# Performance work log

Hardware: AMD Instinct MI355X
Metric: run time of the kernel (lower is better)

Reference implementation:

```python
import jax, jax.numpy as jnp
import numpy as np

DIM = 192
HEADS = 6
POS_DIM = 12  # (dim//4)//4
EPS = 1e-5


def _ln(x, g, b):
    m = jnp.mean(x, -1, keepdims=True)
    v = jnp.var(x, -1, keepdims=True)
    return (x - m) / jnp.sqrt(v + EPS) * g + b


def setup_inputs() -> dict:
    key = jax.random.key(0)
    ks = jax.random.split(key, 20)
    B_, N = 256, 256
    s = 0.02
    inp = {
        "x": jax.random.normal(ks[0], (B_, N, DIM), jnp.float32),
        "mask": jax.random.normal(ks[1], (64, N, N), jnp.float32),
        "w_qkv": jax.random.normal(ks[2], (DIM, 3 * DIM), jnp.float32) * s,
        "b_qkv": jnp.zeros((3 * DIM,), jnp.float32),
        "w_proj": jax.random.normal(ks[3], (DIM, DIM), jnp.float32) * s,
        "b_proj": jnp.zeros((DIM,), jnp.float32),
        "pw0": jax.random.normal(ks[4], (2, POS_DIM), jnp.float32) * s,
        "pb0": jnp.zeros((POS_DIM,), jnp.float32),
        "g1": jnp.ones((POS_DIM,), jnp.float32),
        "be1": jnp.zeros((POS_DIM,), jnp.float32),
        "w1": jax.random.normal(ks[5], (POS_DIM, POS_DIM), jnp.float32) * s,
        "b1": jnp.zeros((POS_DIM,), jnp.float32),
        "g2": jnp.ones((POS_DIM,), jnp.float32),
        "be2": jnp.zeros((POS_DIM,), jnp.float32),
        "w2": jax.random.normal(ks[6], (POS_DIM, POS_DIM), jnp.float32) * s,
        "b2": jnp.zeros((POS_DIM,), jnp.float32),
        "g3": jnp.ones((POS_DIM,), jnp.float32),
        "be3": jnp.zeros((POS_DIM,), jnp.float32),
        "w3": jax.random.normal(ks[7], (POS_DIM, HEADS), jnp.float32) * s,
        "b3": jnp.zeros((HEADS,), jnp.float32),
        "H": 16,
        "W": 16,
    }
    return inp


def reference(x, mask, w_qkv, b_qkv, w_proj, b_proj, pw0, pb0, g1, be1, w1, b1,
              g2, be2, w2, b2, g3, be3, w3, b3, H, W):
    B_, N, C = x.shape
    d = C // HEADS
    scale = d ** (-0.5)
    qkv = (x @ w_qkv + b_qkv).reshape(B_, N, 3, HEADS, d)
    q, k, v = qkv[:, :, 0], qkv[:, :, 1], qkv[:, :, 2]  # [B_, N, h, d]
    attn = jnp.einsum('bnhd,bmhd->bhnm', q * scale, k)

    # dynamic position bias: MLP over relative coordinate offsets
    ph = jnp.arange(1 - H, H)
    pw = jnp.arange(1 - W, W)
    biases = jnp.stack(jnp.meshgrid(ph, pw, indexing='ij')).reshape(2, -1).T.astype(x.dtype)  # [(2H-1)(2W-1), 2]
    pos = biases @ pw0 + pb0
    pos = jax.nn.relu(_ln(pos, g1, be1)) @ w1 + b1
    pos = jax.nn.relu(_ln(pos, g2, be2)) @ w2 + b2
    pos = jax.nn.relu(_ln(pos, g3, be3)) @ w3 + b3  # [(2H-1)(2W-1), heads]

    coords = jnp.stack(jnp.meshgrid(jnp.arange(H), jnp.arange(W), indexing='ij')).reshape(2, -1)  # [2, N]
    rel = coords[:, :, None] - coords[:, None, :]  # [2, N, N]
    rpi = (rel[0] + H - 1) * (2 * W - 1) + (rel[1] + W - 1)  # [N, N]
    rpb = pos[rpi]  # gather -> [N, N, heads]
    attn = attn + jnp.transpose(rpb, (2, 0, 1))[None]

    nP = mask.shape[0]
    attn = attn.reshape(B_ // nP, nP, HEADS, N, N) + mask[None, :, None]
    attn = jax.nn.softmax(attn.reshape(B_, HEADS, N, N), axis=-1)

    out = jnp.einsum('bhnm,bmhd->bnhd', attn, v).reshape(B_, N, C)
    out = out @ w_proj + b_proj
    return out
```

## Files before the change

### kernel.cpp

```cpp
#include <hip/hip_runtime.h>
#include <hip/hip_bf16.h>
#include <math.h>

typedef __bf16 bf16;
typedef __bf16 bf16x8 __attribute__((ext_vector_type(8)));
typedef __bf16 bf16x4 __attribute__((ext_vector_type(4)));
typedef float  f32x4  __attribute__((ext_vector_type(4)));
typedef float  f32x16 __attribute__((ext_vector_type(16)));
typedef _Float16 f16x8 __attribute__((ext_vector_type(8)));

#define MFMA(a, b, c)   __builtin_amdgcn_mfma_f32_16x16x32_bf16((a), (b), (c), 0, 0, 0)
#define MFMA32(a, b, c) __builtin_amdgcn_mfma_f32_32x32x16_bf16((a), (b), (c), 0, 0, 0)
#define LOG2E 1.4426950408889634f

union U8 { unsigned u[4]; bf16x8 v; };

__global__ void precast_kernel(const float* __restrict__ w_qkv,
                               const float* __restrict__ w_proj,
                               bf16* __restrict__ wqT, bf16* __restrict__ wpT) {
  int idx = blockIdx.x * 256 + threadIdx.x;
  if (idx < 576 * 192) {
    int c = idx / 192, k = idx % 192;
    wqT[idx] = (bf16)w_qkv[k * 576 + c];
  } else {
    int i2 = idx - 576 * 192;
    if (i2 < 192 * 192) {
      int c = i2 / 192, k = i2 % 192;
      wpT[i2] = (bf16)w_proj[k * 192 + c];
    }
  }
}

__global__ void pos_mlp_kernel(
    const float* __restrict__ pw0, const float* __restrict__ pb0,
    const float* __restrict__ g1,  const float* __restrict__ be1,
    const float* __restrict__ w1,  const float* __restrict__ b1,
    const float* __restrict__ g2,  const float* __restrict__ be2,
    const float* __restrict__ w2,  const float* __restrict__ b2,
    const float* __restrict__ g3,  const float* __restrict__ be3,
    const float* __restrict__ w3,  const float* __restrict__ b3,
    float* __restrict__ pos_out) {
  int i = blockIdx.x * blockDim.x + threadIdx.x;
  if (i >= 961) return;
  float bh = (float)(i / 31) - 15.0f;
  float bw = (float)(i % 31) - 15.0f;
  float xv[12];
#pragma unroll
  for (int j = 0; j < 12; j++) xv[j] = bh * pw0[j] + bw * pw0[12 + j] + pb0[j];
  const float* G[3]  = {g1, g2, g3};
  const float* BE[3] = {be1, be2, be3};
  const float* W[3]  = {w1, w2, w3};
  const float* BB[3] = {b1, b2, b3};
#pragma unroll
  for (int s = 0; s < 3; s++) {
    float m = 0.f;
#pragma unroll
    for (int j = 0; j < 12; j++) m += xv[j];
    m *= (1.0f / 12.0f);
    float v = 0.f;
#pragma unroll
    for (int j = 0; j < 12; j++) { float d = xv[j] - m; v += d * d; }
    v *= (1.0f / 12.0f);
    float inv = 1.0f / sqrtf(v + 1e-5f);
    float y[12];
#pragma unroll
    for (int j = 0; j < 12; j++) {
      float t = (xv[j] - m) * inv * G[s][j] + BE[s][j];
      y[j] = t > 0.f ? t : 0.f;
    }
    int oc = (s == 2) ? 6 : 12;
    float on[12];
    for (int c = 0; c < oc; c++) {
      float acc = BB[s][c];
#pragma unroll
      for (int j = 0; j < 12; j++) acc += y[j] * W[s][j * oc + c];
      on[c] = acc;
    }
    for (int c = 0; c < 12; c++) xv[c] = (c < oc) ? on[c] : 0.f;
  }
  for (int hh = 0; hh < 6; hh++) pos_out[hh * 961 + i] = xv[hh];
}

__global__ void pos32_build_kernel(const float* __restrict__ posg,
                                   bf16* __restrict__ pos32g) {
  int rd = blockIdx.x, h = blockIdx.y;
  int t = threadIdx.x;
  for (int e = t; e < 512; e += 256) {
    int L = e >> 3, j = e & 7;
    int qh = L & 15;
    int hi = L >> 5;
    int idx = rd * 31 + qh - ((j & 3) + 8 * (j >> 2) + 4 * hi) + 15;
    pos32g[((h * 31 + rd) * 64 + L) * 8 + j] = (bf16)(posg[h * 961 + idx] * LOG2E);
  }
}

__global__ __launch_bounds__(256) void maskprep_kernel(
    const float* __restrict__ mask, _Float16* __restrict__ maskp) {
  size_t e = ((size_t)blockIdx.x * 256 + threadIdx.x) * 2;
  int j  = (int)(e & 15);
  int L  = (int)((e >> 4) & 63);
  int mt = (int)((e >> 10) & 7);
  int qt = (int)((e >> 13) & 7);
  int s  = (int)(e >> 16);
  int q  = qt * 32 + (L & 31);
  int m  = mt * 32 + 16 * (j >> 3) + 8 * ((j >> 2) & 1) + 4 * (L >> 5) + (j & 3);
  const float* src = mask + ((size_t)s * 256 + q) * 256 + m;
  maskp[e]     = (_Float16)(src[0] * LOG2E);
  maskp[e + 1] = (_Float16)(src[1] * LOG2E);
}

#define SMEM_G (192 * 200 * 2)

__global__ __launch_bounds__(256) void qkv_gemm_kernel(
    const float* __restrict__ x, const bf16* __restrict__ wqT,
    const float* __restrict__ b_qkv, bf16* __restrict__ qw,
    bf16* __restrict__ kw, bf16* __restrict__ vwT) {
  extern __shared__ char smem[];
  bf16* wt = (bf16*)smem;
  const int tid = threadIdx.x;
  const int lane = tid & 63, w = tid >> 6;
  const int cI = lane & 15, gI = lane >> 4;
  const int row0 = blockIdx.x * 128 + w * 32;
  const int b = blockIdx.x >> 1;
  const float QSCALE = 0.17677669529663687f * LOG2E;

  bf16x8 afr[2][6];
#pragma unroll
  for (int rt = 0; rt < 2; rt++) {
#pragma unroll
    for (int kk = 0; kk < 6; kk++) {
      const float* p = x + (size_t)(row0 + rt * 16 + cI) * 192 + kk * 32 + gI * 8;
      float4 f0 = *(const float4*)p;
      float4 f1 = *(const float4*)(p + 4);
      bf16x8 a;
      a[0] = (bf16)f0.x; a[1] = (bf16)f0.y; a[2] = (bf16)f0.z; a[3] = (bf16)f0.w;
      a[4] = (bf16)f1.x; a[5] = (bf16)f1.y; a[6] = (bf16)f1.z; a[7] = (bf16)f1.w;
      afr[rt][kk] = a;
    }
  }

#pragma unroll
  for (int mat = 0; mat < 3; mat++) {
    __syncthreads();
#pragma unroll
    for (int it = 0; it < 18; it++) {
      int idx = it * 256 + tid;
      int c = idx / 24, ch = idx % 24;
      bf16x8 v8 = *(const bf16x8*)(wqT + (size_t)(mat * 192 + c) * 192 + ch * 8);
      *(bf16x8*)(wt + c * 200 + ch * 8) = v8;
    }
    __syncthreads();
#pragma unroll
    for (int ct = 0; ct < 12; ct++) {
      bf16x8 wfr[6];
#pragma unroll
      for (int kk = 0; kk < 6; kk++)
        wfr[kk] = *(const bf16x8*)(wt + (ct * 16 + cI) * 200 + kk * 32 + gI * 8);
      if (mat < 2) {
        f32x4 bv4 = *(const f32x4*)(b_qkv + mat * 192 + ct * 16 + gI * 4);
        bf16* dst = (mat == 0) ? qw : kw;
#pragma unroll
        for (int rt = 0; rt < 2; rt++) {
          f32x4 acc = {0.f, 0.f, 0.f, 0.f};
#pragma unroll
          for (int kk = 0; kk < 6; kk++) acc = MFMA(wfr[kk], afr[rt][kk], acc);
          int n = (row0 + rt * 16 + cI) & 255;
          int c0 = ct * 16 + gI * 4;
          int h = c0 >> 5, d0 = c0 & 31;
          bf16x4 o4;
          if (mat == 0) {
#pragma unroll
            for (int r = 0; r < 4; r++) o4[r] = (bf16)((acc[r] + bv4[r]) * QSCALE);
          } else {
#pragma unroll
            for (int r = 0; r < 4; r++) o4[r] = (bf16)(acc[r] + bv4[r]);
          }
          *(bf16x4*)(dst + ((size_t)(b * 6 + h) * 256 + n) * 32 + d0) = o4;
        }
      } else {
        float bv = b_qkv[384 + ct * 16 + cI];
        int c = ct * 16 + cI, h = c >> 5, d = c & 31;
#pragma unroll
        for (int rt = 0; rt < 2; rt++) {
          f32x4 acc = {0.f, 0.f, 0.f, 0.f};
#pragma unroll
          for (int kk = 0; kk < 6; kk++) acc = MFMA(afr[rt][kk], wfr[kk], acc);
          int n0 = ((row0 + rt * 16) & 255) + gI * 4;
          bf16x4 o4;
#pragma unroll
          for (int r = 0; r < 4; r++) o4[r] = (bf16)(acc[r] + bv);
          *(bf16x4*)(vwT + ((size_t)(b * 6 + h) * 32 + d) * 256 + n0) = o4;
        }
      }
    }
  }
}

__global__ __launch_bounds__(256, 4) void attn_kernel(
    const bf16* __restrict__ qw, const bf16* __restrict__ kw,
    const bf16* __restrict__ vwT, const _Float16* __restrict__ maskp,
    const bf16* __restrict__ pos32g, bf16* __restrict__ ctx) {
  const int tid = threadIdx.x;
  const int bid = blockIdx.x;
  const int s_ = bid & 63, j_ = bid >> 6;
  const int g_ = j_ & 3, h = j_ >> 2;
  const int b = g_ * 64 + s_;

  const bf16* qb = qw  + (size_t)(b * 6 + h) * 8192;
  const bf16* kb = kw  + (size_t)(b * 6 + h) * 8192;
  const bf16* vb = vwT + (size_t)(b * 6 + h) * 8192;
  const bf16* pg = pos32g + (size_t)h * (31 * 512);

  const int lane = tid & 63, w = tid >> 6;
  const int q5 = lane & 31, hi = lane >> 5;

  bf16x8 qf[2][2];
#pragma unroll
  for (int sub = 0; sub < 2; sub++) {
    int qa = w * 64 + sub * 32 + q5;
    qf[sub][0] = *(const bf16x8*)(qb + qa * 32 + hi * 8);
    qf[sub][1] = *(const bf16x8*)(qb + qa * 32 + 16 + hi * 8);
  }

  f32x16 o[2];
  float l[2], mr[2];
#pragma unroll
  for (int sub = 0; sub < 2; sub++) {
#pragma unroll
    for (int r = 0; r < 16; r++) o[sub][r] = 0.f;
    l[sub] = 0.f; mr[sub] = -3.0e38f;
  }

  for (int mt = 0; mt < 8; mt++) {
    const int m0 = mt * 32;
    bf16x8 kf0 = *(const bf16x8*)(kb + (m0 + q5) * 32 + hi * 8);
    bf16x8 kf1 = *(const bf16x8*)(kb + (m0 + q5) * 32 + 16 + hi * 8);
    const bf16* vrow = vb + q5 * 256 + m0 + 4 * hi;
    bf16x4 v00 = *(const bf16x4*)(vrow);
    bf16x4 v01 = *(const bf16x4*)(vrow + 8);
    bf16x4 v10 = *(const bf16x4*)(vrow + 16);
    bf16x4 v11 = *(const bf16x4*)(vrow + 24);
    bf16x8 vf0, vf1;
#pragma unroll
    for (int j2 = 0; j2 < 4; j2++) {
      vf0[j2] = v00[j2]; vf0[4 + j2] = v01[j2];
      vf1[j2] = v10[j2]; vf1[4 + j2] = v11[j2];
    }

#pragma unroll
    for (int sub = 0; sub < 2; sub++) {
      const int qa = w * 64 + sub * 32 + q5;
      const int rn = qa >> 4;
      const int rd0 = rn - 2 * mt + 15;
      bf16x8 plo = *(const bf16x8*)(pg + ((rd0)*64 + lane) * 8);
      bf16x8 phi = *(const bf16x8*)(pg + ((rd0 - 1) * 64 + lane) * 8);
      const _Float16* mrow =
          maskp + ((((size_t)s_ * 8 + (w * 2 + sub)) * 8 + mt) * 64 + lane) * 16;
      f16x8 mk0 = *(const f16x8*)(mrow);
      f16x8 mk1 = *(const f16x8*)(mrow + 8);

      f32x16 sa;
#pragma unroll
      for (int r = 0; r < 16; r++) sa[r] = 0.f;
      __builtin_amdgcn_s_setprio(1);
      sa = MFMA32(kf0, qf[sub][0], sa);
      sa = MFMA32(kf1, qf[sub][1], sa);
      __builtin_amdgcn_s_setprio(0);

#pragma unroll
      for (int r = 0; r < 8; r++)  sa[r] += (float)mk0[r] + (float)plo[r];
#pragma unroll
      for (int r = 8; r < 16; r++) sa[r] += (float)mk1[r - 8] + (float)phi[r - 8];

      float t = sa[0];
#pragma unroll
      for (int r = 1; r < 16; r++) t = fmaxf(t, sa[r]);
      t = fmaxf(t, __shfl_xor(t, 32));

      if (!__all(t - mr[sub] <= 8.0f)) {
        float mn = fmaxf(mr[sub], t);
        float fsc = exp2f(mr[sub] - mn);
        mr[sub] = mn;
        l[sub] *= fsc;
#pragma unroll
        for (int r = 0; r < 16; r++) {
          float f = __shfl(fsc, (r & 3) + 8 * (r >> 2) + 4 * hi);
          o[sub][r] *= f;
        }
      }

      float ls = 0.f;
#pragma unroll
      for (int r = 0; r < 16; r++) {
        float p = exp2f(sa[r] - mr[sub]);
        sa[r] = p;
        ls += p;
      }
      ls += __shfl_xor(ls, 32);
      l[sub] += ls;

      unsigned a0, a1, b0, b1, c0, c1, d0, d1;
      asm("v_cvt_pk_bf16_f32 %0, %1, %2" : "=v"(a0) : "v"(sa[0]),  "v"(sa[1]));
      asm("v_cvt_pk_bf16_f32 %0, %1, %2" : "=v"(a1) : "v"(sa[2]),  "v"(sa[3]));
      asm("v_cvt_pk_bf16_f32 %0, %1, %2" : "=v"(b0) : "v"(sa[4]),  "v"(sa[5]));
      asm("v_cvt_pk_bf16_f32 %0, %1, %2" : "=v"(b1) : "v"(sa[6]),  "v"(sa[7]));
      asm("v_cvt_pk_bf16_f32 %0, %1, %2" : "=v"(c0) : "v"(sa[8]),  "v"(sa[9]));
      asm("v_cvt_pk_bf16_f32 %0, %1, %2" : "=v"(c1) : "v"(sa[10]), "v"(sa[11]));
      asm("v_cvt_pk_bf16_f32 %0, %1, %2" : "=v"(d0) : "v"(sa[12]), "v"(sa[13]));
      asm("v_cvt_pk_bf16_f32 %0, %1, %2" : "=v"(d1) : "v"(sa[14]), "v"(sa[15]));
      U8 A1, A2;
      A1.u[0] = a0; A1.u[1] = a1; A1.u[2] = b0; A1.u[3] = b1;
      A2.u[0] = c0; A2.u[1] = c1; A2.u[2] = d0; A2.u[3] = d1;

      __builtin_amdgcn_s_setprio(1);
      o[sub] = MFMA32(A1.v, vf0, o[sub]);
      o[sub] = MFMA32(A2.v, vf1, o[sub]);
      __builtin_amdgcn_s_setprio(0);
    }
  }

#pragma unroll
  for (int sub = 0; sub < 2; sub++) {
    float linv = 1.0f / l[sub];
#pragma unroll
    for (int r = 0; r < 16; r++) {
      int q_local = (r & 3) + 8 * (r >> 2) + 4 * hi;
      float lv = __shfl(linv, q_local);
      int qa = w * 64 + sub * 32 + q_local;
      ctx[((size_t)(b << 8) + qa) * 192 + h * 32 + q5] = (bf16)(o[sub][r] * lv);
    }
  }
}

#define SMEM_C (192 * 200 * 2)

__global__ __launch_bounds__(256) void proj_kernel(
    const bf16* __restrict__ ctx, const bf16* __restrict__ wpT,
    const float* __restrict__ b_proj, float* __restrict__ out) {
  extern __shared__ char smem[];
  bf16* wt = (bf16*)smem;
  const int tid = threadIdx.x;
#pragma unroll
  for (int it = 0; it < 18; it++) {
    int idx = it * 256 + tid;
    int c = idx / 24, ch = idx % 24;
    bf16x8 v8 = *(const bf16x8*)(wpT + (size_t)c * 192 + ch * 8);
    *(bf16x8*)(wt + c * 200 + ch * 8) = v8;
  }
  __syncthreads();
  const int lane = tid & 63, w = tid >> 6;
  const int cI = lane & 15, gI = lane >> 4;
  const int row0 = blockIdx.x * 128 + w * 32;
  bf16x8 afr[2][6];
#pragma unroll
  for (int rt = 0; rt < 2; rt++) {
#pragma unroll
    for (int kk = 0; kk < 6; kk++)
      afr[rt][kk] = *(const bf16x8*)(ctx + (size_t)(row0 + rt * 16 + cI) * 192 +
                                     kk * 32 + gI * 8);
  }
#pragma unroll
  for (int ct = 0; ct < 12; ct++) {
    bf16x8 wfr[6];
#pragma unroll
    for (int kk = 0; kk < 6; kk++)
      wfr[kk] = *(const bf16x8*)(wt + (ct * 16 + cI) * 200 + kk * 32 + gI * 8);
    f32x4 bv4 = *(const f32x4*)(b_proj + ct * 16 + gI * 4);
#pragma unroll
    for (int rt = 0; rt < 2; rt++) {
      f32x4 acc = {0.f, 0.f, 0.f, 0.f};
#pragma unroll
      for (int kk = 0; kk < 6; kk++) acc = MFMA(wfr[kk], afr[rt][kk], acc);
      f32x4 res;
#pragma unroll
      for (int r = 0; r < 4; r++) res[r] = acc[r] + bv4[r];
      *(f32x4*)(out + (size_t)(row0 + rt * 16 + cI) * 192 + ct * 16 + gI * 4) = res;
    }
  }
}

extern "C" void kernel_launch(void* const* d_in, const int* in_sizes, int n_in,
                              void* d_out, int out_size, void* d_ws, size_t ws_size,
                              hipStream_t stream) {
  (void)in_sizes; (void)n_in; (void)out_size; (void)ws_size;
  const float* x      = (const float*)d_in[0];
  const float* mask   = (const float*)d_in[1];
  const float* w_qkv  = (const float*)d_in[2];
  const float* b_qkv  = (const float*)d_in[3];
  const float* w_proj = (const float*)d_in[4];
  const float* b_proj = (const float*)d_in[5];
  const float* pw0    = (const float*)d_in[6];
  const float* pb0    = (const float*)d_in[7];
  const float* g1     = (const float*)d_in[8];
  const float* be1    = (const float*)d_in[9];
  const float* w1     = (const float*)d_in[10];
  const float* b1     = (const float*)d_in[11];
  const float* g2     = (const float*)d_in[12];
  const float* be2    = (const float*)d_in[13];
  const float* w2     = (const float*)d_in[14];
  const float* b2     = (const float*)d_in[15];
  const float* g3     = (const float*)d_in[16];
  const float* be3    = (const float*)d_in[17];
  const float* w3     = (const float*)d_in[18];
  const float* b3     = (const float*)d_in[19];

  char* ws = (char*)d_ws;
  float* posw   = (float*)ws;
  bf16*  wqT    = (bf16*)(ws + 24576);
  bf16*  wpT    = (bf16*)(ws + 245760);
  bf16*  pos32g = (bf16*)(ws + 319488);
  bf16*  qw     = (bf16*)(ws + 516096);
  bf16*  kw     = (bf16*)(ws + 25681920);
  bf16*  vwT    = (bf16*)(ws + 50847744);
  bf16*  ctx    = (bf16*)(ws + 76013568);
  _Float16* maskp = (_Float16*)d_out;
  float* outp   = (float*)d_out;

  hipFuncSetAttribute((const void*)qkv_gemm_kernel,
                      hipFuncAttributeMaxDynamicSharedMemorySize, SMEM_G);
  hipFuncSetAttribute((const void*)proj_kernel,
                      hipFuncAttributeMaxDynamicSharedMemorySize, SMEM_C);

  precast_kernel<<<dim3(576), dim3(256), 0, stream>>>(w_qkv, w_proj, wqT, wpT);
  pos_mlp_kernel<<<dim3(4), dim3(256), 0, stream>>>(
      pw0, pb0, g1, be1, w1, b1, g2, be2, w2, b2, g3, be3, w3, b3, posw);
  pos32_build_kernel<<<dim3(31, 6), dim3(256), 0, stream>>>(posw, pos32g);
  maskprep_kernel<<<dim3(8192), dim3(256), 0, stream>>>(mask, maskp);
  qkv_gemm_kernel<<<dim3(512), dim3(256), SMEM_G, stream>>>(
      x, wqT, b_qkv, qw, kw, vwT);
  attn_kernel<<<dim3(1536), dim3(256), 0, stream>>>(
      qw, kw, vwT, maskp, pos32g, ctx);
  proj_kernel<<<dim3(512), dim3(256), SMEM_C, stream>>>(
      ctx, wpT, b_proj, outp);
}
```

Measured before the change: 138.9 us.

## Merge prep kernels into one launch, drop proj LDS staging, relax attn occupancy

Combines the weight precast, positional MLP, pos32 build and mask prep into one megaprep kernel, going from four launches to one. Block 0 computes the position bias in shared memory while the other blocks cast weights and rearrange the mask. The projection kernel now reads transposed weights straight from global memory (relying on cache) instead of staging them in LDS. The attention kernel's launch bound drops from 4 to 3 waves, giving it more registers. The single-block pos path is serial and may become the critical path of the prep kernel.

Result: slower. 169.6 us (+22.1%).

```diff
diff --git a/kernel.cpp b/kernel.cpp
--- a/kernel.cpp
+++ b/kernel.cpp
@@ -15,23 +15,9 @@
 
 union U8 { unsigned u[4]; bf16x8 v; };
 
-__global__ void precast_kernel(const float* __restrict__ w_qkv,
-                               const float* __restrict__ w_proj,
-                               bf16* __restrict__ wqT, bf16* __restrict__ wpT) {
-  int idx = blockIdx.x * 256 + threadIdx.x;
-  if (idx < 576 * 192) {
-    int c = idx / 192, k = idx % 192;
-    wqT[idx] = (bf16)w_qkv[k * 576 + c];
-  } else {
-    int i2 = idx - 576 * 192;
-    if (i2 < 192 * 192) {
-      int c = i2 / 192, k = i2 % 192;
-      wpT[i2] = (bf16)w_proj[k * 192 + c];
-    }
-  }
-}
-
-__global__ void pos_mlp_kernel(
+__global__ __launch_bounds__(256) void megaprep_kernel(
+    const float* __restrict__ w_qkv, const float* __restrict__ w_proj,
+    const float* __restrict__ mask,
     const float* __restrict__ pw0, const float* __restrict__ pb0,
     const float* __restrict__ g1,  const float* __restrict__ be1,
     const float* __restrict__ w1,  const float* __restrict__ b1,
@@ -39,74 +25,95 @@
     const float* __restrict__ w2,  const float* __restrict__ b2,
     const float* __restrict__ g3,  const float* __restrict__ be3,
     const float* __restrict__ w3,  const float* __restrict__ b3,
-    float* __restrict__ pos_out) {
-  int i = blockIdx.x * blockDim.x + threadIdx.x;
-  if (i >= 961) return;
-  float bh = (float)(i / 31) - 15.0f;
-  float bw = (float)(i % 31) - 15.0f;
-  float xv[12];
-#pragma unroll
-  for (int j = 0; j < 12; j++) xv[j] = bh * pw0[j] + bw * pw0[12 + j] + pb0[j];
-  const float* G[3]  = {g1, g2, g3};
-  const float* BE[3] = {be1, be2, be3};
-  const float* W[3]  = {w1, w2, w3};
-  const float* BB[3] = {b1, b2, b3};
-#pragma unroll
-  for (int s = 0; s < 3; s++) {
-    float m = 0.f;
-#pragma unroll
-    for (int j = 0; j < 12; j++) m += xv[j];
-    m *= (1.0f / 12.0f);
-    float v = 0.f;
-#pragma unroll
-    for (int j = 0; j < 12; j++) { float d = xv[j] - m; v += d * d; }
-    v *= (1.0f / 12.0f);
-    float inv = 1.0f / sqrtf(v + 1e-5f);
-    float y[12];
-#pragma unroll
-    for (int j = 0; j < 12; j++) {
-      float t = (xv[j] - m) * inv * G[s][j] + BE[s][j];
-      y[j] = t > 0.f ? t : 0.f;
-    }
-    int oc = (s == 2) ? 6 : 12;
-    float on[12];
-    for (int c = 0; c < oc; c++) {
-      float acc = BB[s][c];
-#pragma unroll
-      for (int j = 0; j < 12; j++) acc += y[j] * W[s][j * oc + c];
-      on[c] = acc;
-    }
-    for (int c = 0; c < 12; c++) xv[c] = (c < oc) ? on[c] : 0.f;
-  }
-  for (int hh = 0; hh < 6; hh++) pos_out[hh * 961 + i] = xv[hh];
-}
-
-__global__ void pos32_build_kernel(const float* __restrict__ posg,
-                                   bf16* __restrict__ pos32g) {
-  int rd = blockIdx.x, h = blockIdx.y;
-  int t = threadIdx.x;
-  for (int e = t; e < 512; e += 256) {
-    int L = e >> 3, j = e & 7;
-    int qh = L & 15;
-    int hi = L >> 5;
-    int idx = rd * 31 + qh - ((j & 3) + 8 * (j >> 2) + 4 * hi) + 15;
-    pos32g[((h * 31 + rd) * 64 + L) * 8 + j] = (bf16)(posg[h * 961 + idx] * LOG2E);
-  }
-}
-
-__global__ __launch_bounds__(256) void maskprep_kernel(
-    const float* __restrict__ mask, _Float16* __restrict__ maskp) {
-  size_t e = ((size_t)blockIdx.x * 256 + threadIdx.x) * 2;
-  int j  = (int)(e & 15);
-  int L  = (int)((e >> 4) & 63);
-  int mt = (int)((e >> 10) & 7);
-  int qt = (int)((e >> 13) & 7);
-  int s  = (int)(e >> 16);
-  int q  = qt * 32 + (L & 31);
-  int m  = mt * 32 + 16 * (j >> 3) + 8 * ((j >> 2) & 1) + 4 * (L >> 5) + (j & 3);
-  const float* src = mask + ((size_t)s * 256 + q) * 256 + m;
-  maskp[e]     = (_Float16)(src[0] * LOG2E);
-  maskp[e + 1] = (_Float16)(src[1] * LOG2E);
+    bf16* __restrict__ wqT, bf16* __restrict__ wpT,
+    bf16* __restrict__ pos32g, _Float16* __restrict__ maskp) {
+  __shared__ float posh[961];
+  const int blk = blockIdx.x;
+  const int t = threadIdx.x;
+
+  if (blk == 0) {
+    float outv[4][6];
+    const float* G[3]  = {g1, g2, g3};
+    const float* BE[3] = {be1, be2, be3};
+    const float* W[3]  = {w1, w2, w3};
+    const float* BB[3] = {b1, b2, b3};
+#pragma unroll
+    for (int k = 0; k < 4; k++) {
+      int i = t + k * 256;
+      if (i >= 961) break;
+      float bh = (float)(i / 31) - 15.0f;
+      float bw = (float)(i % 31) - 15.0f;
+      float xv[12];
+#pragma unroll
+      for (int j = 0; j < 12; j++) xv[j] = bh * pw0[j] + bw * pw0[12 + j] + pb0[j];
+#pragma unroll
+      for (int s = 0; s < 3; s++) {
+        float m = 0.f;
+#pragma unroll
+        for (int j = 0; j < 12; j++) m += xv[j];
+        m *= (1.0f / 12.0f);
+        float v = 0.f;
+#pragma unroll
+        for (int j = 0; j < 12; j++) { float d = xv[j] - m; v += d * d; }
+        v *= (1.0f / 12.0f);
+        float inv = 1.0f / sqrtf(v + 1e-5f);
+        float y[12];
+#pragma unroll
+        for (int j = 0; j < 12; j++) {
+          float tt = (xv[j] - m) * inv * G[s][j] + BE[s][j];
+          y[j] = tt > 0.f ? tt : 0.f;
+        }
+        int oc = (s == 2) ? 6 : 12;
+        float on[12];
+        for (int c = 0; c < oc; c++) {
+          float acc = BB[s][c];
+#pragma unroll
+          for (int j = 0; j < 12; j++) acc += y[j] * W[s][j * oc + c];
+          on[c] = acc;
+        }
+        for (int c = 0; c < 12; c++) xv[c] = (c < oc) ? on[c] : 0.f;
+      }
+#pragma unroll
+      for (int hh = 0; hh < 6; hh++) outv[k][hh] = xv[hh];
+    }
+    for (int h = 0; h < 6; h++) {
+      __syncthreads();
+#pragma unroll
+      for (int k = 0; k < 4; k++) {
+        int i = t + k * 256;
+        if (i < 961) posh[i] = outv[k][h];
+      }
+      __syncthreads();
+      for (int e = t; e < 15872; e += 256) {
+        int rd = e >> 9, idx2 = e & 511;
+        int L = idx2 >> 3, j = idx2 & 7;
+        int index = rd * 31 + (L & 15) - ((j & 3) + 8 * (j >> 2) + 4 * (L >> 5)) + 15;
+        pos32g[h * 15872 + e] = (bf16)(posh[index] * LOG2E);
+      }
+    }
+  } else if (blk <= 576) {
+    int idx = (blk - 1) * 256 + t;
+    if (idx < 576 * 192) {
+      int c = idx / 192, k = idx % 192;
+      wqT[idx] = (bf16)w_qkv[k * 576 + c];
+    } else {
+      int i2 = idx - 576 * 192;
+      int c = i2 / 192, k = i2 % 192;
+      wpT[i2] = (bf16)w_proj[k * 192 + c];
+    }
+  } else {
+    size_t e = ((size_t)(blk - 577) * 256 + t) * 2;
+    int j  = (int)(e & 15);
+    int L  = (int)((e >> 4) & 63);
+    int mt = (int)((e >> 10) & 7);
+    int qt = (int)((e >> 13) & 7);
+    int s  = (int)(e >> 16);
+    int q  = qt * 32 + (L & 31);
+    int m  = mt * 32 + 16 * (j >> 3) + 8 * ((j >> 2) & 1) + 4 * (L >> 5) + (j & 3);
+    const float* src = mask + ((size_t)s * 256 + q) * 256 + m;
+    maskp[e]     = (_Float16)(src[0] * LOG2E);
+    maskp[e + 1] = (_Float16)(src[1] * LOG2E);
+  }
 }
 
 #define SMEM_G (192 * 200 * 2)
@@ -196,7 +203,7 @@
   }
 }
 
-__global__ __launch_bounds__(256, 4) void attn_kernel(
+__global__ __launch_bounds__(256, 3) void attn_kernel(
     const bf16* __restrict__ qw, const bf16* __restrict__ kw,
     const bf16* __restrict__ vwT, const _Float16* __restrict__ maskp,
     const bf16* __restrict__ pos32g, bf16* __restrict__ ctx) {
@@ -252,8 +259,8 @@
       const int qa = w * 64 + sub * 32 + q5;
       const int rn = qa >> 4;
       const int rd0 = rn - 2 * mt + 15;
-      bf16x8 plo = *(const bf16x8*)(pg + ((rd0)*64 + lane) * 8);
-      bf16x8 phi = *(const bf16x8*)(pg + ((rd0 - 1) * 64 + lane) * 8);
+      bf16x8 plo = *(const bf16x8*)(pg + ((size_t)rd0 * 64 + lane) * 8);
+      bf16x8 phi = *(const bf16x8*)(pg + ((size_t)(rd0 - 1) * 64 + lane) * 8);
       const _Float16* mrow =
           maskp + ((((size_t)s_ * 8 + (w * 2 + sub)) * 8 + mt) * 64 + lane) * 16;
       f16x8 mk0 = *(const f16x8*)(mrow);
@@ -268,9 +275,9 @@
       __builtin_amdgcn_s_setprio(0);
 
 #pragma unroll
-      for (int r = 0; r < 8; r++)  sa[r] += (float)mk0[r] + (float)plo[r];
-#pragma unroll
-      for (int r = 8; r < 16; r++) sa[r] += (float)mk1[r - 8] + (float)phi[r - 8];
+      for (int r = 0; r < 8; r++)  sa[r]     += (float)mk0[r] + (float)plo[r];
+#pragma unroll
+      for (int r = 8; r < 16; r++) sa[r]     += (float)mk1[r - 8] + (float)phi[r - 8];
 
       float t = sa[0];
 #pragma unroll
@@ -332,22 +339,10 @@
   }
 }
 
-#define SMEM_C (192 * 200 * 2)
-
 __global__ __launch_bounds__(256) void proj_kernel(
     const bf16* __restrict__ ctx, const bf16* __restrict__ wpT,
     const float* __restrict__ b_proj, float* __restrict__ out) {
-  extern __shared__ char smem[];
-  bf16* wt = (bf16*)smem;
   const int tid = threadIdx.x;
-#pragma unroll
-  for (int it = 0; it < 18; it++) {
-    int idx = it * 256 + tid;
-    int c = idx / 24, ch = idx % 24;
-    bf16x8 v8 = *(const bf16x8*)(wpT + (size_t)c * 192 + ch * 8);
-    *(bf16x8*)(wt + c * 200 + ch * 8) = v8;
-  }
-  __syncthreads();
   const int lane = tid & 63, w = tid >> 6;
   const int cI = lane & 15, gI = lane >> 4;
   const int row0 = blockIdx.x * 128 + w * 32;
@@ -364,7 +359,7 @@
     bf16x8 wfr[6];
 #pragma unroll
     for (int kk = 0; kk < 6; kk++)
-      wfr[kk] = *(const bf16x8*)(wt + (ct * 16 + cI) * 200 + kk * 32 + gI * 8);
+      wfr[kk] = *(const bf16x8*)(wpT + (size_t)(ct * 16 + cI) * 192 + kk * 32 + gI * 8);
     f32x4 bv4 = *(const f32x4*)(b_proj + ct * 16 + gI * 4);
 #pragma unroll
     for (int rt = 0; rt < 2; rt++) {
@@ -405,31 +400,27 @@
   const float* b3     = (const float*)d_in[19];
 
   char* ws = (char*)d_ws;
-  float* posw   = (float*)ws;
-  bf16*  wqT    = (bf16*)(ws + 24576);
-  bf16*  wpT    = (bf16*)(ws + 245760);
-  bf16*  pos32g = (bf16*)(ws + 319488);
-  bf16*  qw     = (bf16*)(ws + 516096);
-  bf16*  kw     = (bf16*)(ws + 25681920);
-  bf16*  vwT    = (bf16*)(ws + 50847744);
-  bf16*  ctx    = (bf16*)(ws + 76013568);
+  bf16*  wqT    = (bf16*)(ws);
+  bf16*  wpT    = (bf16*)(ws + 221184);
+  bf16*  pos32g = (bf16*)(ws + 294912);
+  bf16*  qw     = (bf16*)(ws + 485376);
+  bf16*  kw     = (bf16*)(ws + 25651200);
+  bf16*  vwT    = (bf16*)(ws + 50817024);
+  bf16*  ctx    = (bf16*)(ws + 75982848);
   _Float16* maskp = (_Float16*)d_out;
   float* outp   = (float*)d_out;
 
   hipFuncSetAttribute((const void*)qkv_gemm_kernel,
                       hipFuncAttributeMaxDynamicSharedMemorySize, SMEM_G);
-  hipFuncSetAttribute((const void*)proj_kernel,
-                      hipFuncAttributeMaxDynamicSharedMemorySize, SMEM_C);
-
-  precast_kernel<<<dim3(576), dim3(256), 0, stream>>>(w_qkv, w_proj, wqT, wpT);
-  pos_mlp_kernel<<<dim3(4), dim3(256), 0, stream>>>(
-      pw0, pb0, g1, be1, w1, b1, g2, be2, w2, b2, g3, be3, w3, b3, posw);
-  pos32_build_kernel<<<dim3(31, 6), dim3(256), 0, stream>>>(posw, pos32g);
-  maskprep_kernel<<<dim3(8192), dim3(256), 0, stream>>>(mask, maskp);
+
+  megaprep_kernel<<<dim3(8769), dim3(256), 0, stream>>>(
+      w_qkv, w_proj, mask,
+      pw0, pb0, g1, be1, w1, b1, g2, be2, w2, b2, g3, be3, w3, b3,
+      wqT, wpT, pos32g, maskp);
   qkv_gemm_kernel<<<dim3(512), dim3(256), SMEM_G, stream>>>(
       x, wqT, b_qkv, qw, kw, vwT);
   attn_kernel<<<dim3(1536), dim3(256), 0, stream>>>(
       qw, kw, vwT, maskp, pos32g, ctx);
-  proj_kernel<<<dim3(512), dim3(256), SMEM_C, stream>>>(
+  proj_kernel<<<dim3(512), dim3(256), 0, stream>>>(
       ctx, wpT, b_proj, outp);
 }
```
